# Kernel tuning notes

Hardware: AMD Instinct MI355X
Metric: run time of the kernel (lower is better)

The kernel has to match this reference:

```python
import jax, jax.numpy as jnp
import numpy as np

EPS = 1e-5
GROUPS = 32

def octree_conv(x, neigh, W, b):
    # x: [N, Cin], neigh: [N, 27] (-1 => empty neighbor), W: [27, Cin, Cout]
    N = x.shape[0]
    xp = jnp.concatenate([x, jnp.zeros((1, x.shape[1]), x.dtype)], axis=0)  # zero row for empties
    idx = jnp.where(neigh < 0, N, neigh)
    g = xp[idx]                                # [N, 27, Cin] gathered neighbor features
    return jnp.einsum('nkc,kcd->nd', g, W) + b

def octree_group_norm(x, weight, bias, groups=GROUPS):
    # Normalize each group over all non-empty nodes and the channels in the group.
    N, C = x.shape
    xg = x.reshape(N, groups, C // groups)
    mean = jnp.mean(xg, axis=(0, 2), keepdims=True)
    var = jnp.mean(jnp.square(xg - mean), axis=(0, 2), keepdims=True)
    xn = ((xg - mean) * jax.lax.rsqrt(var + EPS)).reshape(N, C)
    return xn * weight + bias

def setup_inputs() -> dict:
    key = jax.random.key(0)
    ks = jax.random.split(key, 8)
    N, Cin, Cmid, Cout, K = 50000, 128, 128, 32, 27
    data = jax.random.normal(ks[0], (N, Cin), dtype=jnp.float32)
    neigh = jax.random.randint(ks[1], (N, K), 0, N, dtype=jnp.int64)
    W1 = jax.random.normal(ks[2], (K, Cin, Cmid), dtype=jnp.float32) * (1.0 / np.sqrt(K * Cin))
    b1 = jnp.zeros((Cmid,), dtype=jnp.float32)
    gn_w = jnp.ones((Cmid,), dtype=jnp.float32)
    gn_b = jnp.zeros((Cmid,), dtype=jnp.float32)
    W2 = jax.random.normal(ks[3], (K, Cmid, Cout), dtype=jnp.float32) * (1.0 / np.sqrt(K * Cmid))
    b2 = jnp.zeros((Cout,), dtype=jnp.float32)
    return {"data": data, "neigh": neigh, "W1": W1, "b1": b1,
            "gn_w": gn_w, "gn_b": gn_b, "W2": W2, "b2": b2}

def reference(data, neigh, W1, b1, gn_w, gn_b, W2, b2):
    x = octree_conv(data, neigh, W1, b1)          # conv1: in -> mid
    x = octree_group_norm(x, gn_w, gn_b)          # GroupNorm over nodes per group
    x = jax.nn.silu(x)                            # SiLU
    x = octree_conv(x, neigh, W2, b2)             # conv2: mid -> out
    return x
```

## Files before the change

### kernel.cpp

```cpp
#include <hip/hip_runtime.h>
#include <stdint.h>

#define N_NODES 50000
#define CIN 128
#define CMID 128
#define COUT 32
#define KNB 27
#define EPSV 1e-5f

typedef __attribute__((ext_vector_type(4))) float f4v;
typedef __attribute__((ext_vector_type(8))) short s8v;
typedef __attribute__((ext_vector_type(4))) short s4v;

__device__ __forceinline__ unsigned short f2bf(float f) {
  union { float f; uint32_t u; } v; v.f = f;
  return (unsigned short)((v.u + 0x7FFFu + ((v.u >> 16) & 1u)) >> 16);
}
__device__ __forceinline__ float bf2f(short s) {
  return __uint_as_float(((uint32_t)(uint16_t)s) << 16);
}

__device__ __forceinline__ f4v mfma16(s8v a, s8v b, f4v c) {
  return __builtin_amdgcn_mfma_f32_16x16x32_bf16(a, b, c, 0, 0, 0);
}

__device__ __forceinline__ void gload_lds16(const void* g, void* lds) {
  __builtin_amdgcn_global_load_lds(
      (const __attribute__((address_space(1))) uint32_t*)(uintptr_t)g,
      (__attribute__((address_space(3))) uint32_t*)(uint32_t)(uintptr_t)lds,
      16, 0, 0);
}

__device__ __forceinline__ bool neigh_is64(const void* neigh) {
  const int* p = (const int*)neigh;
  int ok = 1;
#pragma unroll
  for (int i = 0; i < 16; ++i) {
    int hi = p[2 * i + 1];
    if (hi != 0 && hi != -1) ok = 0;
  }
  return ok != 0;
}

__global__ __launch_bounds__(256) void k_transpose(
    const void* __restrict__ neigh, int* __restrict__ neighT)
{
  __shared__ int tT[KNB][257];
  const int r0 = blockIdx.x * 256;
  const bool is64 = neigh_is64(neigh);
  const int tid = threadIdx.x;
  for (int e = tid; e < 256 * KNB; e += 256) {
    int r = e / KNB, k = e - r * KNB;
    if (r0 + r < N_NODES) {
      long long v = is64 ? ((const long long*)neigh)[(size_t)r0 * KNB + e]
                         : (long long)((const int*)neigh)[(size_t)r0 * KNB + e];
      tT[k][r] = (v < 0) ? N_NODES : (int)v;
    }
  }
  __syncthreads();
  for (int e = tid; e < KNB * 256; e += 256) {
    int k = e >> 8, r = e & 255;
    if (r0 + r < N_NODES) neighT[(size_t)k * N_NODES + r0 + r] = tT[k][r];
  }
}

__global__ __launch_bounds__(256) void k_prep_x(
    const float* __restrict__ data, short* __restrict__ xb,
    float* __restrict__ gsums)
{
  const int TOT0 = (N_NODES + 1) * (CIN / 4);
  int gtid = blockIdx.x * 256 + threadIdx.x;
  int stride = gridDim.x * 256;
  for (int i = gtid; i < TOT0; i += stride) {
    int row = i >> 5, c4 = i & 31;
    s4v o = {};
    if (row < N_NODES) {
      f4v v = *(const f4v*)(data + (size_t)row * CIN + c4 * 4);
      o[0] = (short)f2bf(v[0]); o[1] = (short)f2bf(v[1]);
      o[2] = (short)f2bf(v[2]); o[3] = (short)f2bf(v[3]);
    }
    *(s4v*)(xb + (size_t)row * CIN + c4 * 4) = o;
  }
  if (gtid < 64) gsums[gtid] = 0.0f;
}

__global__ __launch_bounds__(256) void k_prep_w(
    const float* __restrict__ W1, const float* __restrict__ W2,
    short* __restrict__ wt1f, short* __restrict__ wt2f)
{
  __shared__ short T1[128][136];
  __shared__ short T2[32][136];
  const int k = blockIdx.x;
  const int tid = threadIdx.x;

  const float* w1p = W1 + (size_t)k * (CIN * CMID);
  for (int i = tid; i < CIN * CMID / 4; i += 256) {
    int c = i >> 5, d4 = i & 31;
    f4v v = *(const f4v*)(w1p + c * CMID + d4 * 4);
#pragma unroll
    for (int j = 0; j < 4; ++j) T1[d4 * 4 + j][c] = (short)f2bf(v[j]);
  }
  const float* w2p = W2 + (size_t)k * (CMID * COUT);
  for (int i = tid; i < CMID * COUT / 4; i += 256) {
    int c = i >> 3, d4 = i & 7;
    f4v v = *(const f4v*)(w2p + c * COUT + d4 * 4);
#pragma unroll
    for (int j = 0; j < 4; ++j) T2[d4 * 4 + j][c] = (short)f2bf(v[j]);
  }
  __syncthreads();

  for (int q = tid; q < 2048; q += 256) {
    int l = q & 63, n = (q >> 6) & 7, kc = q >> 9;
    int cin0 = kc * 32 + ((l >> 4) << 3), cout = n * 16 + (l & 15);
    s8v v = *(const s8v*)&T1[cout][cin0];
    *(s8v*)(wt1f + ((size_t)k * 2048 + q) * 8) = v;
  }
  for (int q = tid; q < 512; q += 256) {
    int l = q & 63, n = (q >> 6) & 1, kc = q >> 7;
    int cin0 = kc * 32 + ((l >> 4) << 3), cout = n * 16 + (l & 15);
    s8v v = *(const s8v*)&T2[cout][cin0];
    *(s8v*)(wt2f + ((size_t)k * 512 + q) * 8) = v;
  }
}

__global__ __launch_bounds__(256, 2) void k_conv1(
    const short* __restrict__ xb, const int* __restrict__ neighT,
    const short* __restrict__ wt1f, short* __restrict__ x1p)
{
  __shared__ short Bs[2][8192];
  __shared__ short As[4][2][2048];
  const int tid = threadIdx.x;
  const int l = tid & 63, w = tid >> 6;
  const int bx = blockIdx.x;
  const int kh = (bx >= 391) ? 1 : 0;
  const int rb = kh ? bx - 391 : bx;
  const int rw = rb * 128 + w * 32;
  const int k0 = kh ? 13 : 0, k1 = kh ? 27 : 13;
  const int lr = l & 15, lho = l >> 4;
  const int l8 = l >> 3, ls = l & 7;

  f4v acc[2][8] = {};
  int idx[4], idxn[4];
  s8v ga[4];

  auto loadIdx = [&](int* id, int k) {
#pragma unroll
    for (int q = 0; q < 4; ++q) {
      int r = rw + q * 8 + l8; if (r >= N_NODES) r = N_NODES - 1;
      id[q] = neighT[(size_t)k * N_NODES + r];
    }
  };
  auto stageB = [&](int buf, int k, int h) {
    const short* src = wt1f + ((size_t)(k * 4 + h * 2) * 8) * 512 + l * 8;
#pragma unroll
    for (int j = 0; j < 4; ++j)
      gload_lds16(src + (w * 4 + j) * 512, &Bs[buf][(w * 4 + j) * 512]);
  };
  auto gatherA = [&](const int* id, int h) {
#pragma unroll
    for (int q = 0; q < 4; ++q)
      ga[q] = *(const s8v*)(xb + (size_t)id[q] * CIN + h * 64 + ls * 8);
  };
  auto writeA = [&](int buf) {
#pragma unroll
    for (int q = 0; q < 4; ++q)
      *(s8v*)&As[w][buf][(q * 8 + l8) * 64 + ((ls ^ l8) * 8)] = ga[q];
  };
  auto compute = [&](int cb) {
#pragma unroll
    for (int kc = 0; kc < 2; ++kc) {
      s8v af[2];
#pragma unroll
      for (int rg = 0; rg < 2; ++rg) {
        int row = rg * 16 + lr;
        af[rg] = *(const s8v*)&As[w][cb][row * 64 + (((kc * 4 + lho) ^ (lr & 7)) * 8)];
      }
#pragma unroll
      for (int n = 0; n < 8; ++n) {
        s8v bf = *(const s8v*)&Bs[cb][(kc * 8 + n) * 512 + l * 8];
        acc[0][n] = mfma16(af[0], bf, acc[0][n]);
        acc[1][n] = mfma16(af[1], bf, acc[1][n]);
      }
    }
  };

  loadIdx(idx, k0);
  stageB(0, k0, 0);
  gatherA(idx, 0);
  __syncthreads();
  writeA(0);

  int cur = 0;
  for (int k = k0; k < k1; ++k) {
    const bool more = (k + 1 < k1);
    stageB(cur ^ 1, k, 1);
    gatherA(idx, 1);
    if (more) loadIdx(idxn, k + 1);
    compute(cur);
    __syncthreads();
    writeA(cur ^ 1);
    cur ^= 1;
    if (more) { stageB(cur ^ 1, k + 1, 0); gatherA(idxn, 0); }
    compute(cur);
    __syncthreads();
    if (more) {
      writeA(cur ^ 1);
#pragma unroll
      for (int q = 0; q < 4; ++q) idx[q] = idxn[q];
    }
    cur ^= 1;
  }

  short* xp = x1p + (size_t)kh * N_NODES * CMID;
#pragma unroll
  for (int rg = 0; rg < 2; ++rg) {
#pragma unroll
    for (int j = 0; j < 4; ++j) {
      int grow = rw + rg * 16 + lho * 4 + j;
      if (grow < N_NODES) {
#pragma unroll
        for (int n = 0; n < 8; ++n)
          xp[(size_t)grow * CMID + n * 16 + lr] = (short)f2bf(acc[rg][n][j]);
      }
    }
  }
}

__global__ __launch_bounds__(256) void k_sum(
    const short* __restrict__ x1p, const float* __restrict__ b1,
    float* __restrict__ gsums)
{
  __shared__ float sh[64];
  const int tid = threadIdx.x;
  if (tid < 64) sh[tid] = 0.0f;
  __syncthreads();
  const int g = tid & 31;
  const short* p0 = x1p;
  const short* p1 = x1p + (size_t)N_NODES * CMID;
  f4v bv = *(const f4v*)(b1 + g * 4);
  float s = 0.f, ss = 0.f;
  for (int r = blockIdx.x * 8 + (tid >> 5); r < N_NODES; r += gridDim.x * 8) {
    s4v v0 = *(const s4v*)(p0 + (size_t)r * CMID + g * 4);
    s4v v1 = *(const s4v*)(p1 + (size_t)r * CMID + g * 4);
#pragma unroll
    for (int e = 0; e < 4; ++e) {
      float x = bf2f(v0[e]) + bf2f(v1[e]) + bv[e];
      s += x; ss += x * x;
    }
  }
  s += __shfl_xor(s, 32); ss += __shfl_xor(ss, 32);
  if ((tid & 32) == 0) { atomicAdd(&sh[g], s); atomicAdd(&sh[32 + g], ss); }
  __syncthreads();
  if (tid < 64) atomicAdd(&gsums[tid], sh[tid]);
}

__global__ __launch_bounds__(256) void k_gnsilu(
    const short* __restrict__ x1p, const float* __restrict__ b1,
    const float* __restrict__ gsums, const float* __restrict__ gn_w,
    const float* __restrict__ gn_b, short* __restrict__ xnb)
{
  const float invc = 1.0f / (N_NODES * 4.0f);
  const short* p0 = x1p;
  const short* p1 = x1p + (size_t)N_NODES * CMID;
  int gtid = blockIdx.x * 256 + threadIdx.x;
  int stride = gridDim.x * 256;
  const int TOT = (N_NODES + 1) * (CMID / 4);
  for (int i = gtid; i < TOT; i += stride) {
    int row = i >> 5, g = i & 31;
    s4v o = {};
    if (row < N_NODES) {
      float mean = gsums[g] * invc;
      float var = gsums[32 + g] * invc - mean * mean;
      float rs = rsqrtf(var + EPSV);
      s4v v0 = *(const s4v*)(p0 + (size_t)row * CMID + g * 4);
      s4v v1 = *(const s4v*)(p1 + (size_t)row * CMID + g * 4);
      f4v bv = *(const f4v*)(b1 + g * 4);
      f4v wv = *(const f4v*)(gn_w + g * 4);
      f4v gv = *(const f4v*)(gn_b + g * 4);
#pragma unroll
      for (int e = 0; e < 4; ++e) {
        float x = bf2f(v0[e]) + bf2f(v1[e]) + bv[e];
        float xn = (x - mean) * rs * wv[e] + gv[e];
        float y = xn / (1.0f + __expf(-xn));
        o[e] = (short)f2bf(y);
      }
    }
    *(s4v*)(xnb + (size_t)row * CMID + g * 4) = o;
  }
}

__global__ __launch_bounds__(256, 4) void k_conv2(
    const short* __restrict__ xnb, const int* __restrict__ neighT,
    const short* __restrict__ wt2f, float* __restrict__ x2p)
{
  __shared__ short Bs[2][2048];
  __shared__ short As[4][2][2048];
  const int tid = threadIdx.x;
  const int l = tid & 63, w = tid >> 6;
  const int bx = blockIdx.x;
  const int kh = (bx >= 391) ? 1 : 0;
  const int rb = kh ? bx - 391 : bx;
  const int rw = rb * 128 + w * 32;
  const int k0 = kh ? 13 : 0, k1 = kh ? 27 : 13;
  const int lr = l & 15, lho = l >> 4;
  const int l8 = l >> 3, ls = l & 7;

  f4v acc[2][2] = {};
  int idx[4], idxn[4];
  s8v ga[4];

  auto loadIdx = [&](int* id, int k) {
#pragma unroll
    for (int q = 0; q < 4; ++q) {
      int r = rw + q * 8 + l8; if (r >= N_NODES) r = N_NODES - 1;
      id[q] = neighT[(size_t)k * N_NODES + r];
    }
  };
  auto stageB = [&](int buf, int k, int h) {
    const short* src = wt2f + ((size_t)(k * 4 + h * 2) * 2) * 512 + l * 8;
    gload_lds16(src + w * 512, &Bs[buf][w * 512]);
  };
  auto gatherA = [&](const int* id, int h) {
#pragma unroll
    for (int q = 0; q < 4; ++q)
      ga[q] = *(const s8v*)(xnb + (size_t)id[q] * CMID + h * 64 + ls * 8);
  };
  auto writeA = [&](int buf) {
#pragma unroll
    for (int q = 0; q < 4; ++q)
      *(s8v*)&As[w][buf][(q * 8 + l8) * 64 + ((ls ^ l8) * 8)] = ga[q];
  };
  auto compute = [&](int cb) {
#pragma unroll
    for (int kc = 0; kc < 2; ++kc) {
      s8v af[2];
#pragma unroll
      for (int rg = 0; rg < 2; ++rg) {
        int row = rg * 16 + lr;
        af[rg] = *(const s8v*)&As[w][cb][row * 64 + (((kc * 4 + lho) ^ (lr & 7)) * 8)];
      }
#pragma unroll
      for (int n = 0; n < 2; ++n) {
        s8v bf = *(const s8v*)&Bs[cb][(kc * 2 + n) * 512 + l * 8];
        acc[0][n] = mfma16(af[0], bf, acc[0][n]);
        acc[1][n] = mfma16(af[1], bf, acc[1][n]);
      }
    }
  };

  loadIdx(idx, k0);
  stageB(0, k0, 0);
  gatherA(idx, 0);
  __syncthreads();
  writeA(0);

  int cur = 0;
  for (int k = k0; k < k1; ++k) {
    const bool more = (k + 1 < k1);
    stageB(cur ^ 1, k, 1);
    gatherA(idx, 1);
    if (more) loadIdx(idxn, k + 1);
    compute(cur);
    __syncthreads();
    writeA(cur ^ 1);
    cur ^= 1;
    if (more) { stageB(cur ^ 1, k + 1, 0); gatherA(idxn, 0); }
    compute(cur);
    __syncthreads();
    if (more) {
      writeA(cur ^ 1);
#pragma unroll
      for (int q = 0; q < 4; ++q) idx[q] = idxn[q];
    }
    cur ^= 1;
  }

  float* xp = x2p + (size_t)kh * N_NODES * COUT;
#pragma unroll
  for (int rg = 0; rg < 2; ++rg) {
#pragma unroll
    for (int j = 0; j < 4; ++j) {
      int grow = rw + rg * 16 + lho * 4 + j;
      if (grow < N_NODES) {
#pragma unroll
        for (int n = 0; n < 2; ++n)
          xp[(size_t)grow * COUT + n * 16 + lr] = acc[rg][n][j];
      }
    }
  }
}

__global__ __launch_bounds__(256) void k_fin(
    const float* __restrict__ x2p, const float* __restrict__ b2,
    float* __restrict__ out)
{
  int i = blockIdx.x * 256 + threadIdx.x;
  const int TOT = N_NODES * COUT / 4;
  if (i < TOT) {
    int c4 = i & 7;
    f4v a = *(const f4v*)(x2p + (size_t)i * 4);
    f4v b = *(const f4v*)(x2p + (size_t)N_NODES * COUT + (size_t)i * 4);
    f4v bias = *(const f4v*)(b2 + c4 * 4);
    f4v o = a + b + bias;
    *(f4v*)(out + (size_t)i * 4) = o;
  }
}

extern "C" void kernel_launch(void* const* d_in, const int* in_sizes, int n_in,
                              void* d_out, int out_size, void* d_ws, size_t ws_size,
                              hipStream_t stream) {
  const float* data = (const float*)d_in[0];
  const void* neigh = d_in[1];
  const float* W1   = (const float*)d_in[2];
  const float* b1   = (const float*)d_in[3];
  const float* gn_w = (const float*)d_in[4];
  const float* gn_b = (const float*)d_in[5];
  const float* W2   = (const float*)d_in[6];
  const float* b2   = (const float*)d_in[7];

  char* p = (char*)d_ws;
  short* xb   = (short*)p; p += (size_t)(N_NODES + 1) * CIN * 2;
  float* x2p  = (float*)xb;
  short* wt1f = (short*)p; p += (size_t)KNB * CMID * CIN * 2;
  short* wt2f = (short*)p; p += (size_t)KNB * COUT * CMID * 2;
  short* x1p  = (short*)p; p += (size_t)2 * N_NODES * CMID * 2;
  short* xnb  = (short*)p; p += (size_t)(N_NODES + 1) * CMID * 2;
  int*   neighT = (int*)p; p += (size_t)KNB * N_NODES * 4;
  float* gsums = (float*)p;

  k_transpose<<<(N_NODES + 255) / 256, 256, 0, stream>>>(neigh, neighT);
  k_prep_x<<<2048, 256, 0, stream>>>(data, xb, gsums);
  k_prep_w<<<KNB, 256, 0, stream>>>(W1, W2, wt1f, wt2f);
  k_conv1<<<782, 256, 0, stream>>>(xb, neighT, wt1f, x1p);
  k_sum<<<391, 256, 0, stream>>>(x1p, b1, gsums);
  k_gnsilu<<<2048, 256, 0, stream>>>(x1p, b1, gsums, gn_w, gn_b, xnb);
  k_conv2<<<782, 256, 0, stream>>>(xnb, neighT, wt2f, x2p);
  k_fin<<<(N_NODES * COUT / 4 + 255) / 256, 256, 0, stream>>>(x2p, b2, (float*)d_out);
}
```

Baseline: 243.6 us.

## Reorder conv2 as dense projection then neighbor gather-sum of bf16 partials

Conv2 now runs as a dense per-node product of xnb with every neighbor's weight slice into a bf16 buffer (32 channels per neighbor slot), followed by a gather-add over neighbors. Gathering 32-wide outputs replaces gathering 128-wide inputs, and the work is split into two halves so the projection buffer fits in the reused workspace. This removes the gather-heavy MFMA loop and the final reduction kernel. In exchange it adds an extra bf16 rounding of the partial products and writes and reads a large intermediate buffer.

```diff
diff --git a/kernel.cpp b/kernel.cpp
--- a/kernel.cpp
+++ b/kernel.cpp
@@ -116,10 +116,11 @@
     *(s8v*)(wt1f + ((size_t)k * 2048 + q) * 8) = v;
   }
   for (int q = tid; q < 512; q += 256) {
-    int l = q & 63, n = (q >> 6) & 1, kc = q >> 7;
-    int cin0 = kc * 32 + ((l >> 4) << 3), cout = n * 16 + (l & 15);
+    int l = q & 63, kc = (q >> 6) & 3, t2 = q >> 8;
+    int cin0 = kc * 32 + ((l >> 4) << 3), cout = t2 * 16 + (l & 15);
     s8v v = *(const s8v*)&T2[cout][cin0];
-    *(s8v*)(wt2f + ((size_t)k * 512 + q) * 8) = v;
+    int chunk = (2 * k + t2) * 4 + kc;
+    *(s8v*)(wt2f + ((size_t)chunk << 9) + l * 8) = v;
   }
 }
 
@@ -264,146 +265,106 @@
   const short* p1 = x1p + (size_t)N_NODES * CMID;
   int gtid = blockIdx.x * 256 + threadIdx.x;
   int stride = gridDim.x * 256;
-  const int TOT = (N_NODES + 1) * (CMID / 4);
+  const int TOT = N_NODES * (CMID / 4);
   for (int i = gtid; i < TOT; i += stride) {
     int row = i >> 5, g = i & 31;
-    s4v o = {};
-    if (row < N_NODES) {
-      float mean = gsums[g] * invc;
-      float var = gsums[32 + g] * invc - mean * mean;
-      float rs = rsqrtf(var + EPSV);
-      s4v v0 = *(const s4v*)(p0 + (size_t)row * CMID + g * 4);
-      s4v v1 = *(const s4v*)(p1 + (size_t)row * CMID + g * 4);
-      f4v bv = *(const f4v*)(b1 + g * 4);
-      f4v wv = *(const f4v*)(gn_w + g * 4);
-      f4v gv = *(const f4v*)(gn_b + g * 4);
-#pragma unroll
-      for (int e = 0; e < 4; ++e) {
-        float x = bf2f(v0[e]) + bf2f(v1[e]) + bv[e];
-        float xn = (x - mean) * rs * wv[e] + gv[e];
-        float y = xn / (1.0f + __expf(-xn));
-        o[e] = (short)f2bf(y);
+    float mean = gsums[g] * invc;
+    float var = gsums[32 + g] * invc - mean * mean;
+    float rs = rsqrtf(var + EPSV);
+    s4v v0 = *(const s4v*)(p0 + (size_t)row * CMID + g * 4);
+    s4v v1 = *(const s4v*)(p1 + (size_t)row * CMID + g * 4);
+    f4v bv = *(const f4v*)(b1 + g * 4);
+    f4v wv = *(const f4v*)(gn_w + g * 4);
+    f4v gv = *(const f4v*)(gn_b + g * 4);
+    s4v o;
+#pragma unroll
+    for (int e = 0; e < 4; ++e) {
+      float x = bf2f(v0[e]) + bf2f(v1[e]) + bv[e];
+      float xn = (x - mean) * rs * wv[e] + gv[e];
+      float y = xn / (1.0f + __expf(-xn));
+      o[e] = (short)f2bf(y);
+    }
+    *(s4v*)(xnb + (size_t)row * CMID + g * 4) = o;
+  }
+}
+
+template<int T0, int NT>
+__global__ __launch_bounds__(256) void k_proj(
+    const short* __restrict__ xnb, const short* __restrict__ wt2f,
+    short* __restrict__ cbuf)
+{
+  const int tid = threadIdx.x;
+  const int l = tid & 63, w = tid >> 6;
+  const int rw = blockIdx.x * 128 + w * 32;
+  const int lr = l & 15, lho = l >> 4;
+  const int NC = NT * 16;
+
+  s8v a[2][4];
+#pragma unroll
+  for (int rs = 0; rs < 2; ++rs) {
+    int row = rw + rs * 16 + lr; if (row >= N_NODES) row = N_NODES - 1;
+    const short* p = xnb + (size_t)row * CMID + lho * 8;
+#pragma unroll
+    for (int kc = 0; kc < 4; ++kc) a[rs][kc] = *(const s8v*)(p + kc * 32);
+  }
+
+#pragma unroll 2
+  for (int t = 0; t < NT; ++t) {
+    const short* wp = wt2f + ((size_t)((T0 + t) * 4) << 9) + l * 8;
+    s8v bf[4];
+#pragma unroll
+    for (int kc = 0; kc < 4; ++kc) bf[kc] = *(const s8v*)(wp + (kc << 9));
+    f4v acc[2] = {};
+#pragma unroll
+    for (int kc = 0; kc < 4; ++kc) {
+      acc[0] = mfma16(a[0][kc], bf[kc], acc[0]);
+      acc[1] = mfma16(a[1][kc], bf[kc], acc[1]);
+    }
+#pragma unroll
+    for (int rs = 0; rs < 2; ++rs) {
+#pragma unroll
+      for (int j = 0; j < 4; ++j) {
+        int row = rw + rs * 16 + lho * 4 + j;
+        if (row < N_NODES)
+          cbuf[(size_t)row * NC + t * 16 + lr] = (short)f2bf(acc[rs][j]);
       }
     }
-    *(s4v*)(xnb + (size_t)row * CMID + g * 4) = o;
-  }
-}
-
-__global__ __launch_bounds__(256, 4) void k_conv2(
-    const short* __restrict__ xnb, const int* __restrict__ neighT,
-    const short* __restrict__ wt2f, float* __restrict__ x2p)
-{
-  __shared__ short Bs[2][2048];
-  __shared__ short As[4][2][2048];
-  const int tid = threadIdx.x;
-  const int l = tid & 63, w = tid >> 6;
-  const int bx = blockIdx.x;
-  const int kh = (bx >= 391) ? 1 : 0;
-  const int rb = kh ? bx - 391 : bx;
-  const int rw = rb * 128 + w * 32;
-  const int k0 = kh ? 13 : 0, k1 = kh ? 27 : 13;
-  const int lr = l & 15, lho = l >> 4;
-  const int l8 = l >> 3, ls = l & 7;
-
-  f4v acc[2][2] = {};
-  int idx[4], idxn[4];
-  s8v ga[4];
-
-  auto loadIdx = [&](int* id, int k) {
-#pragma unroll
-    for (int q = 0; q < 4; ++q) {
-      int r = rw + q * 8 + l8; if (r >= N_NODES) r = N_NODES - 1;
-      id[q] = neighT[(size_t)k * N_NODES + r];
-    }
-  };
-  auto stageB = [&](int buf, int k, int h) {
-    const short* src = wt2f + ((size_t)(k * 4 + h * 2) * 2) * 512 + l * 8;
-    gload_lds16(src + w * 512, &Bs[buf][w * 512]);
-  };
-  auto gatherA = [&](const int* id, int h) {
-#pragma unroll
-    for (int q = 0; q < 4; ++q)
-      ga[q] = *(const s8v*)(xnb + (size_t)id[q] * CMID + h * 64 + ls * 8);
-  };
-  auto writeA = [&](int buf) {
-#pragma unroll
-    for (int q = 0; q < 4; ++q)
-      *(s8v*)&As[w][buf][(q * 8 + l8) * 64 + ((ls ^ l8) * 8)] = ga[q];
-  };
-  auto compute = [&](int cb) {
-#pragma unroll
-    for (int kc = 0; kc < 2; ++kc) {
-      s8v af[2];
-#pragma unroll
-      for (int rg = 0; rg < 2; ++rg) {
-        int row = rg * 16 + lr;
-        af[rg] = *(const s8v*)&As[w][cb][row * 64 + (((kc * 4 + lho) ^ (lr & 7)) * 8)];
-      }
-#pragma unroll
-      for (int n = 0; n < 2; ++n) {
-        s8v bf = *(const s8v*)&Bs[cb][(kc * 2 + n) * 512 + l * 8];
-        acc[0][n] = mfma16(af[0], bf, acc[0][n]);
-        acc[1][n] = mfma16(af[1], bf, acc[1][n]);
-      }
-    }
-  };
-
-  loadIdx(idx, k0);
-  stageB(0, k0, 0);
-  gatherA(idx, 0);
-  __syncthreads();
-  writeA(0);
-
-  int cur = 0;
-  for (int k = k0; k < k1; ++k) {
-    const bool more = (k + 1 < k1);
-    stageB(cur ^ 1, k, 1);
-    gatherA(idx, 1);
-    if (more) loadIdx(idxn, k + 1);
-    compute(cur);
-    __syncthreads();
-    writeA(cur ^ 1);
-    cur ^= 1;
-    if (more) { stageB(cur ^ 1, k + 1, 0); gatherA(idxn, 0); }
-    compute(cur);
-    __syncthreads();
-    if (more) {
-      writeA(cur ^ 1);
-#pragma unroll
-      for (int q = 0; q < 4; ++q) idx[q] = idxn[q];
-    }
-    cur ^= 1;
-  }
-
-  float* xp = x2p + (size_t)kh * N_NODES * COUT;
-#pragma unroll
-  for (int rg = 0; rg < 2; ++rg) {
-#pragma unroll
-    for (int j = 0; j < 4; ++j) {
-      int grow = rw + rg * 16 + lho * 4 + j;
-      if (grow < N_NODES) {
-#pragma unroll
-        for (int n = 0; n < 2; ++n)
-          xp[(size_t)grow * COUT + n * 16 + lr] = acc[rg][n][j];
-      }
-    }
-  }
-}
-
-__global__ __launch_bounds__(256) void k_fin(
-    const float* __restrict__ x2p, const float* __restrict__ b2,
-    float* __restrict__ out)
-{
-  int i = blockIdx.x * 256 + threadIdx.x;
-  const int TOT = N_NODES * COUT / 4;
-  if (i < TOT) {
-    int c4 = i & 7;
-    f4v a = *(const f4v*)(x2p + (size_t)i * 4);
-    f4v b = *(const f4v*)(x2p + (size_t)N_NODES * COUT + (size_t)i * 4);
-    f4v bias = *(const f4v*)(b2 + c4 * 4);
-    f4v o = a + b + bias;
-    *(f4v*)(out + (size_t)i * 4) = o;
-  }
+  }
+}
+
+template<int INIT, int KC, int KSTART>
+__global__ __launch_bounds__(256) void k_gather2(
+    const short* __restrict__ cbuf, const void* __restrict__ neigh,
+    const float* __restrict__ b2, float* __restrict__ out)
+{
+  const int tid = threadIdx.x;
+  const int n = blockIdx.x * 32 + (tid >> 3);
+  const int l8 = tid & 7;
+  if (n >= N_NODES) return;
+  const bool is64 = neigh_is64(neigh);
+  const int NC = KC * 32;
+
+  int id[KC]; float msk[KC];
+#pragma unroll
+  for (int k = 0; k < KC; ++k) {
+    long long v = is64 ? ((const long long*)neigh)[(size_t)n * KNB + KSTART + k]
+                       : (long long)((const int*)neigh)[(size_t)n * KNB + KSTART + k];
+    msk[k] = (v >= 0) ? 1.0f : 0.0f;
+    id[k] = (v >= 0) ? (int)v : 0;
+  }
+  f4v acc;
+  if (INIT) acc = *(const f4v*)(b2 + l8 * 4);
+  else      acc = *(const f4v*)(out + (size_t)n * COUT + l8 * 4);
+  s4v cv[KC];
+#pragma unroll
+  for (int k = 0; k < KC; ++k)
+    cv[k] = *(const s4v*)(cbuf + (size_t)id[k] * NC + k * 32 + l8 * 4);
+#pragma unroll
+  for (int k = 0; k < KC; ++k) {
+#pragma unroll
+    for (int e = 0; e < 4; ++e) acc[e] += msk[k] * bf2f(cv[k][e]);
+  }
+  *(f4v*)(out + (size_t)n * COUT + l8 * 4) = acc;
 }
 
 extern "C" void kernel_launch(void* const* d_in, const int* in_sizes, int n_in,
@@ -419,13 +380,15 @@
   const float* b2   = (const float*)d_in[7];
 
   char* p = (char*)d_ws;
+  char* r0 = p;
   short* xb   = (short*)p; p += (size_t)(N_NODES + 1) * CIN * 2;
-  float* x2p  = (float*)xb;
   short* wt1f = (short*)p; p += (size_t)KNB * CMID * CIN * 2;
-  short* wt2f = (short*)p; p += (size_t)KNB * COUT * CMID * 2;
+  int*   neighT = (int*)p; p += (size_t)KNB * N_NODES * 4;
   short* x1p  = (short*)p; p += (size_t)2 * N_NODES * CMID * 2;
+  short* cbuf = (short*)r0;
+  p = r0 + (size_t)N_NODES * 448 * 2;
   short* xnb  = (short*)p; p += (size_t)(N_NODES + 1) * CMID * 2;
-  int*   neighT = (int*)p; p += (size_t)KNB * N_NODES * 4;
+  short* wt2f = (short*)p; p += (size_t)54 * 4 * 64 * 8 * 2;
   float* gsums = (float*)p;
 
   k_transpose<<<(N_NODES + 255) / 256, 256, 0, stream>>>(neigh, neighT);
@@ -433,7 +396,9 @@
   k_prep_w<<<KNB, 256, 0, stream>>>(W1, W2, wt1f, wt2f);
   k_conv1<<<782, 256, 0, stream>>>(xb, neighT, wt1f, x1p);
   k_sum<<<391, 256, 0, stream>>>(x1p, b1, gsums);
-  k_gnsilu<<<2048, 256, 0, stream>>>(x1p, b1, gsums, gn_w, gn_b, xnb);
-  k_conv2<<<782, 256, 0, stream>>>(xnb, neighT, wt2f, x2p);
-  k_fin<<<(N_NODES * COUT / 4 + 255) / 256, 256, 0, stream>>>(x2p, b2, (float*)d_out);
-}
+  k_gnsilu<<<1563, 256, 0, stream>>>(x1p, b1, gsums, gn_w, gn_b, xnb);
+  k_proj<0, 28><<<391, 256, 0, stream>>>(xnb, wt2f, cbuf);
+  k_gather2<1, 14, 0><<<1563, 256, 0, stream>>>(cbuf, neigh, b2, (float*)d_out);
+  k_proj<28, 26><<<391, 256, 0, stream>>>(xnb, wt2f, cbuf);
+  k_gather2<0, 13, 14><<<1563, 256, 0, stream>>>(cbuf, neigh, b2, (float*)d_out);
+}
```

After: 280.3 us. 1.15x slower.
